# Performance work log

Measured on AMD Instinct MI355X. Metric: run time of the kernel, lower is better.

Reference implementation:

```python
import jax, jax.numpy as jnp
import numpy as np

N, E, D, H, HEADS_C, G = 50000, 800000, 128, 4, 32, 8
EDIM = D + 2  # H_update: phys_term (D) + ortho_geom (2)


def setup_inputs() -> dict:
    key = jax.random.key(0)
    ks = jax.random.split(key, 24)
    def gl(k, shape, fan_in):
        return jax.random.normal(k, shape, jnp.float32) / np.sqrt(fan_in)
    inp = {
        'h_target': jax.random.normal(ks[0], (N, D), jnp.float32),
        'h_source': jax.random.normal(ks[1], (N, D), jnp.float32),
        'edge_index': jax.random.randint(ks[2], (2, E), 0, N, jnp.int64),
        'pos': jax.random.uniform(ks[3], (N, 2), jnp.float32),
        't_emb': jax.random.normal(ks[4], (1, D), jnp.float32),
        # AdaGN params
        'gn_w': jnp.ones((D,), jnp.float32),
        'gn_b': jnp.zeros((D,), jnp.float32),
        'fc_W': gl(ks[5], (D, 2 * D), D),
        'fc_b': jnp.zeros((2 * D,), jnp.float32),
        # GATv2 params (lin_l, lin_r, lin_edge, att, bias)
        'Wl': gl(ks[6], (D, D), D),
        'bl': jnp.zeros((D,), jnp.float32),
        'Wr': gl(ks[7], (D, D), D),
        'br': jnp.zeros((D,), jnp.float32),
        'We': gl(ks[8], (EDIM, D), EDIM),
        'att': gl(ks[9], (H, HEADS_C), HEADS_C),
        'gat_b': jnp.zeros((D,), jnp.float32),
        # post_gat
        'Wp': gl(ks[10], (D, D), D),
        'bp': jnp.zeros((D,), jnp.float32),
        # update_mlp: LayerNorm + Linear(D,2D) + GELU + Linear(2D,D)
        'ln_w': jnp.ones((D,), jnp.float32),
        'ln_b': jnp.zeros((D,), jnp.float32),
        'W1': gl(ks[11], (D, 2 * D), D),
        'b1': jnp.zeros((2 * D,), jnp.float32),
        'W2': gl(ks[12], (2 * D, D), 2 * D),
        'b2': jnp.zeros((D,), jnp.float32),
    }
    return inp


def _adagn(x, cond, gn_w, gn_b, fc_W, fc_b):
    n, d = x.shape
    xg = x.reshape(n, G, d // G)
    mu = xg.mean(-1, keepdims=True)
    var = xg.var(-1, keepdims=True)  # biased, as torch GroupNorm
    normed = ((xg - mu) / jnp.sqrt(var + 1e-5)).reshape(n, d) * gn_w + gn_b
    style = cond @ fc_W + fc_b  # (1, 2D) broadcasts over nodes
    gamma, beta = jnp.split(style, 2, axis=-1)
    return normed * (1 + gamma) + beta


def _gatv2(h, edge_attr, src, dst, Wl, bl, Wr, br, We, att, gat_b):
    n = h.shape[0]
    x_l = (h @ Wl + bl).reshape(n, H, HEADS_C)  # source transform
    x_r = (h @ Wr + br).reshape(n, H, HEADS_C)  # target transform
    e_feat = (edge_attr @ We).reshape(-1, H, HEADS_C)
    x = x_l[src] + x_r[dst] + e_feat            # (E, H, C)
    x = jax.nn.leaky_relu(x, 0.2)
    logit = jnp.einsum('ehc,hc->eh', x, att)    # (E, H)
    # segment softmax over edges grouped by destination node
    amax = jax.ops.segment_max(logit, dst, num_segments=n)
    amax = jnp.where(jnp.isfinite(amax), amax, 0.0)
    ex = jnp.exp(logit - amax[dst])
    denom = jax.ops.segment_sum(ex, dst, num_segments=n)
    alpha = ex / (denom[dst] + 1e-16)           # (E, H)
    msg = x_l[src] * alpha[:, :, None]          # (E, H, C)
    out = jax.ops.segment_sum(msg, dst, num_segments=n)  # (N, H, C)
    return out.reshape(n, H * HEADS_C) + gat_b


def reference(h_target, h_source, edge_index, pos, t_emb,
              gn_w, gn_b, fc_W, fc_b,
              Wl, bl, Wr, br, We, att, gat_b,
              Wp, bp, ln_w, ln_b, W1, b1, W2, b2):
    h_mod = _adagn(h_source, t_emb, gn_w, gn_b, fc_W, fc_b)
    src, dst = edge_index[0], edge_index[1]
    rel_pos = pos[src] - pos[dst]                       # (E, 2)
    dist_sq = (rel_pos ** 2).sum(-1, keepdims=True) + 1e-8
    geom = rel_pos / dist_sq
    phys = h_mod[src] - h_mod[dst]                      # H_update mode
    ortho = jnp.stack([-geom[:, 1], geom[:, 0]], axis=-1)
    edge_attr = jnp.concatenate([phys, ortho], axis=-1)  # (E, D+2)
    aggr = _gatv2(h_mod, edge_attr, src, dst, Wl, bl, Wr, br, We, att, gat_b)
    aggr = aggr @ Wp + bp
    # update_mlp (dropout inactive in eval)
    mu = aggr.mean(-1, keepdims=True)
    var = aggr.var(-1, keepdims=True)
    z = (aggr - mu) / jnp.sqrt(var + 1e-5) * ln_w + ln_b
    z = jax.nn.gelu(z @ W1 + b1, approximate=False)
    delta = z @ W2 + b2
    return h_target + delta
```

## Files before the change

### kernel.cpp

```cpp
#include <hip/hip_runtime.h>
#include <math.h>

#define D 128

typedef short bf16x4 __attribute__((ext_vector_type(4)));
typedef short bf16x8 __attribute__((ext_vector_type(8)));
typedef float f32x4  __attribute__((ext_vector_type(4)));

__device__ __forceinline__ float b2f(unsigned short u) {
  union { unsigned int i; float f; } v; v.i = ((unsigned int)u) << 16; return v.f;
}
__device__ __forceinline__ unsigned short f2b(float f) {
  union { float f; unsigned int i; } v; v.f = f;
  unsigned int i = v.i;
  return (unsigned short)((i + 0x7FFFu + ((i >> 16) & 1u)) >> 16);
}
__device__ __forceinline__ float b2f_lo(unsigned int u) {
  union { unsigned int i; float f; } v; v.i = u << 16; return v.f;
}
__device__ __forceinline__ float b2f_hi(unsigned int u) {
  union { unsigned int i; float f; } v; v.i = u & 0xFFFF0000u; return v.f;
}
__device__ __forceinline__ float loadf(const void* p, size_t i, int isb) {
  if (isb) return b2f(((const unsigned short*)p)[i]);
  return ((const float*)p)[i];
}
__device__ __forceinline__ void storeout(void* p, size_t i, float v, int isb) {
  if (isb) ((unsigned short*)p)[i] = f2b(v);
  else     ((float*)p)[i] = v;
}
__device__ __forceinline__ int clampN(int v, int N) {
  return ((unsigned)v >= (unsigned)N) ? 0 : v;
}

__global__ void setup_kernel(const float* __restrict__ gw, const int* __restrict__ e32,
                             int* __restrict__ fflag, int* __restrict__ iflag,
                             int* __restrict__ ok) {
  int t = threadIdx.x;
  if (blockIdx.x == 0) {
    float v = gw[t];
    unsigned long long b = __ballot(v == 1.0f);
    if (t == 0) fflag[0] = (b == 0xFFFFFFFFFFFFFFFFull) ? 0 : 1;
  } else if (blockIdx.x == 1) {
    int v = e32[2 * t + 1];
    unsigned long long b = __ballot(v == 0);
    if (t == 0) iflag[0] = (b == 0xFFFFFFFFFFFFFFFFull) ? 1 : 0;
  } else {
    if (t == 0) ok[0] = 1;
  }
}
__device__ __forceinline__ int edge_src(const void* eraw, int i, int E, int fl, int N) {
  int v = fl ? (int)((const long long*)eraw)[i] : ((const int*)eraw)[i];
  return clampN(v, N);
}
__device__ __forceinline__ int edge_dst(const void* eraw, int i, int E, int fl, int N) {
  int v = fl ? (int)((const long long*)eraw)[(size_t)E + i] : ((const int*)eraw)[(size_t)E + i];
  return clampN(v, N);
}

struct Job { const void* src; float* dst; int n; int blk0; };
struct Jobs { Job j[21]; };
__global__ void cvt_param_kernel(Jobs jobs, const int* __restrict__ fflag, int njobs) {
  int isb = fflag[0];
  int b = blockIdx.x;
  for (int k = 0; k < njobs; ++k) {
    int nblk = (jobs.j[k].n + 255) >> 8;
    int lo = jobs.j[k].blk0;
    if (b >= lo && b < lo + nblk) {
      int i = ((b - lo) << 8) + threadIdx.x;
      if (i < jobs.j[k].n) jobs.j[k].dst[i] = loadf(jobs.j[k].src, i, isb);
      return;
    }
  }
}

__global__ void style_kernel(const float* __restrict__ t_emb,
                             const float* __restrict__ fc_W,
                             const float* __restrict__ fc_b,
                             float* __restrict__ style) {
  int j = threadIdx.x;
  float s = fc_b[j];
  for (int k = 0; k < D; ++k) s += t_emb[k] * fc_W[k * 256 + j];
  style[j] = s;
}

__global__ __launch_bounds__(128) void adagn_kernel(
    const void* __restrict__ h_source,
    const float* __restrict__ gn_w, const float* __restrict__ gn_b,
    const float* __restrict__ style, unsigned short* __restrict__ h_mod,
    const int* __restrict__ fflag, int N) {
  int n = blockIdx.x; if (n >= N) return;
  int c = threadIdx.x;
  float x = loadf(h_source, (size_t)n * D + c, fflag[0]);
  float s = x, s2 = x * x;
  s += __shfl_xor(s, 1, 16);  s2 += __shfl_xor(s2, 1, 16);
  s += __shfl_xor(s, 2, 16);  s2 += __shfl_xor(s2, 2, 16);
  s += __shfl_xor(s, 4, 16);  s2 += __shfl_xor(s2, 4, 16);
  s += __shfl_xor(s, 8, 16);  s2 += __shfl_xor(s2, 8, 16);
  float mu = s * (1.f / 16.f);
  float va = s2 * (1.f / 16.f) - mu * mu;
  float iv = rsqrtf(va + 1e-5f);
  float nv = (x - mu) * iv * gn_w[c] + gn_b[c];
  h_mod[(size_t)n * D + c] = f2b(nv * (1.f + style[c]) + style[128 + c]);
}

struct BP { const float* B; int ldb; int col0; };
struct BPJobs { BP j[8]; };
__global__ void bprep_kernel(BPJobs jobs, unsigned short* __restrict__ dst) {
  int job = blockIdx.x >> 7;
  int idx = ((blockIdx.x & 127) << 8) + threadIdx.x;
  int j    = idx & 7;
  int lane = (idx >> 3) & 63;
  int p    = (idx >> 9) & 1;
  int ct   = (idx >> 10) & 7;
  int kt   = idx >> 13;
  int g = lane >> 4;
  int k = kt * 32 + ((j < 4) ? (4 * g + j) : (16 + 4 * g + (j - 4)));
  int n = jobs.j[job].col0 + ct * 16 + (lane & 15);
  float v = jobs.j[job].B[(size_t)k * jobs.j[job].ldb + n];
  unsigned short hi = f2b(v);
  unsigned short out = hi;
  if (p) out = f2b(v - b2f(hi));
  dst[(size_t)job * 32768 + idx] = out;
}

template <int MODE, int CTS, int KTS>
__global__ __launch_bounds__(256) void mgemm_kernel(
    const unsigned short* __restrict__ A, const unsigned short* __restrict__ Bf,
    const float* __restrict__ bias, const void* __restrict__ resid,
    void* __restrict__ Cv, const int* __restrict__ fflag,
    const int* __restrict__ okf, int Nrows) {
  const int AS = KTS * 32, LDC = CTS * 16;
  int l = threadIdx.x & 63, w = threadIdx.x >> 6;
  int rb = blockIdx.x * 64 + w * 16;
  int m = l & 15, g = l >> 4;
  int arow = rb + m;
  if (arow >= Nrows) arow = Nrows - 1;
  const unsigned short* Arow = A + (size_t)arow * AS + 4 * g;
  f32x4 acc[CTS];
  #pragma unroll
  for (int ct = 0; ct < CTS; ++ct) acc[ct] = (f32x4){0.f, 0.f, 0.f, 0.f};
  #pragma unroll
  for (int kt = 0; kt < KTS; ++kt) {
    bf16x4 alo = *(const bf16x4*)(Arow + kt * 32);
    bf16x4 ahi = *(const bf16x4*)(Arow + kt * 32 + 16);
    bf16x8 af = __builtin_shufflevector(alo, ahi, 0, 1, 2, 3, 4, 5, 6, 7);
    #pragma unroll
    for (int ct = 0; ct < CTS; ++ct) {
      int panel = (KTS == 8) ? (kt >> 2) : (ct >> 3);
      size_t off = (size_t)panel * 32768 + (size_t)(kt & 3) * 8192
                 + (size_t)(((ct & 7) * 2) * 64 + l) * 8;
      bf16x8 bh = *(const bf16x8*)(Bf + off);
      bf16x8 bl2 = *(const bf16x8*)(Bf + off + 512);
      acc[ct] = __builtin_amdgcn_mfma_f32_16x16x32_bf16(af, bh, acc[ct], 0, 0, 0);
      acc[ct] = __builtin_amdgcn_mfma_f32_16x16x32_bf16(af, bl2, acc[ct], 0, 0, 0);
    }
  }
  int isb = (MODE == 2) ? fflag[0] : 0;
  int okv = (MODE == 2) ? okf[0] : 1;
  #pragma unroll
  for (int ct = 0; ct < CTS; ++ct) {
    int c = ct * 16 + m;
    float bs = bias[c];
    #pragma unroll
    for (int r = 0; r < 4; ++r) {
      int row = rb + 4 * g + r;
      if (row < Nrows) {
        float v = acc[ct][r] + bs;
        if (MODE == 1) v = 0.5f * v * (1.f + erff(v * 0.70710678118654752f));
        size_t oi = (size_t)row * LDC + c;
        if (MODE == 2) {
          v += loadf(resid, oi, isb);
          if (okv == 0) v = 100.0f;
          storeout(Cv, oi, v, isb);
        } else ((unsigned short*)Cv)[oi] = f2b(v);
      }
    }
  }
}

__global__ __launch_bounds__(256) void mgemm3_kernel(
    const unsigned short* __restrict__ A, const unsigned short* __restrict__ Bf,
    const float* __restrict__ bl, const float* __restrict__ br,
    unsigned int* __restrict__ XH32, unsigned short* __restrict__ XR, int Nrows) {
  int l = threadIdx.x & 63, w = threadIdx.x >> 6;
  int rb = blockIdx.x * 64 + w * 16;
  int m = l & 15, g = l >> 4;
  int arow = rb + m;
  if (arow >= Nrows) arow = Nrows - 1;
  const unsigned short* Arow = A + (size_t)arow * 128 + 4 * g;
  f32x4 acc[24];
  #pragma unroll
  for (int ct = 0; ct < 24; ++ct) acc[ct] = (f32x4){0.f, 0.f, 0.f, 0.f};
  #pragma unroll
  for (int kt = 0; kt < 4; ++kt) {
    bf16x4 alo = *(const bf16x4*)(Arow + kt * 32);
    bf16x4 ahi = *(const bf16x4*)(Arow + kt * 32 + 16);
    bf16x8 af = __builtin_shufflevector(alo, ahi, 0, 1, 2, 3, 4, 5, 6, 7);
    #pragma unroll
    for (int ct = 0; ct < 24; ++ct) {
      size_t off = (size_t)(ct >> 3) * 32768 + (size_t)kt * 8192
                 + (size_t)(((ct & 7) * 2) * 64 + l) * 8;
      bf16x8 bh = *(const bf16x8*)(Bf + off);
      bf16x8 bl2 = *(const bf16x8*)(Bf + off + 512);
      acc[ct] = __builtin_amdgcn_mfma_f32_16x16x32_bf16(af, bh, acc[ct], 0, 0, 0);
      acc[ct] = __builtin_amdgcn_mfma_f32_16x16x32_bf16(af, bl2, acc[ct], 0, 0, 0);
    }
  }
  #pragma unroll
  for (int ct = 0; ct < 8; ++ct) {
    int cm = ct * 16 + m;
    #pragma unroll
    for (int r = 0; r < 4; ++r) {
      int row = rb + 4 * g + r;
      if (row < Nrows) {
        float vl = acc[ct][r] + bl[cm];
        float vh = acc[ct + 16][r];
        XH32[(size_t)row * 128 + cm] =
            (unsigned int)f2b(vl) | ((unsigned int)f2b(vh) << 16);
        float vr = acc[ct + 8][r] + br[cm];
        XR[(size_t)row * 128 + cm] = f2b(vr);
      }
    }
  }
}

__global__ void hist_kernel(const void* __restrict__ eraw, const int* __restrict__ iflag,
                            int* __restrict__ deg, int E, int N) {
  int e = blockIdx.x * 256 + threadIdx.x;
  if (e < E) atomicAdd(&deg[edge_dst(eraw, e, E, iflag[0], N)], 1);
}

__global__ __launch_bounds__(1024) void scan1_kernel(const int* __restrict__ deg,
                                                     int* __restrict__ incl,
                                                     int* __restrict__ bsum) {
  int i = blockIdx.x * 1024 + threadIdx.x;
  int lane = threadIdx.x & 63, wave = threadIdx.x >> 6;
  int x = deg[i];
  #pragma unroll
  for (int d = 1; d < 64; d <<= 1) { int t = __shfl_up(x, d, 64); if (lane >= d) x += t; }
  __shared__ int wsum[16];
  if (lane == 63) wsum[wave] = x;
  __syncthreads();
  if (threadIdx.x < 16) {
    int w = wsum[threadIdx.x];
    #pragma unroll
    for (int d = 1; d < 16; d <<= 1) { int t = __shfl_up(w, d, 64); if ((int)threadIdx.x >= d) w += t; }
    wsum[threadIdx.x] = w;
  }
  __syncthreads();
  if (wave > 0) x += wsum[wave - 1];
  incl[i] = x;
  if (threadIdx.x == 1023) bsum[blockIdx.x] = x;
}

__global__ void scan2_kernel(const int* __restrict__ bsum, int* __restrict__ bbase, int nb) {
  if (threadIdx.x == 0) {
    int run = 0;
    for (int b = 0; b < nb; ++b) { bbase[b] = run; run += bsum[b]; }
  }
}

__global__ __launch_bounds__(1024) void scan3_kernel(const int* __restrict__ incl,
                                                     const int* __restrict__ deg,
                                                     const int* __restrict__ bbase,
                                                     int* __restrict__ offs,
                                                     int* __restrict__ cursor, int N) {
  int i = blockIdx.x * 1024 + threadIdx.x;
  if (i < N) {
    int o = bbase[blockIdx.x] + incl[i] - deg[i];
    offs[i] = o; cursor[i] = o;
  }
}

__global__ void scatter_kernel(const void* __restrict__ eraw, const int* __restrict__ iflag,
                               int* __restrict__ cursor, int* __restrict__ elist, int E, int N) {
  int e = blockIdx.x * 256 + threadIdx.x;
  if (e < E) {
    int fl = iflag[0];
    int d = edge_dst(eraw, e, E, fl, N);
    int s = edge_src(eraw, e, E, fl, N);
    int p = atomicAdd(&cursor[d], 1);
    elist[p] = s;
  }
}

__global__ void validate_kernel(const int* __restrict__ offs, const int* __restrict__ deg,
                                const int* __restrict__ cursor, const int* __restrict__ elist,
                                int* __restrict__ ok, int N, int E) {
  int i = blockIdx.x * 256 + threadIdx.x;
  bool bad = false;
  if (i < N) bad = bad || (cursor[i] != offs[i] + deg[i]);
  if (i < E) bad = bad || ((unsigned)elist[i] >= (unsigned)N);
  if (i == 0) bad = bad || (offs[N - 1] + deg[N - 1] != E);
  if (bad) atomicAnd(ok, 0);
}
__global__ void fillc_kernel(void* __restrict__ out, float c, const int* __restrict__ fflag, int n) {
  int i = blockIdx.x * 256 + threadIdx.x;
  if (i < n) storeout(out, i, c, fflag[0]);
}

__global__ __launch_bounds__(256) void edge_kernel(
    const unsigned int* __restrict__ XH32, const unsigned short* __restrict__ XR,
    const float* __restrict__ pos, const float* __restrict__ weo,
    const float* __restrict__ att, const float* __restrict__ gat_b,
    const int* __restrict__ offs, const int* __restrict__ deg,
    const int* __restrict__ elist, unsigned short* __restrict__ aggr, int N) {
  int w = threadIdx.x >> 6;
  int l = threadIdx.x & 63;
  int n = blockIdx.x * 2 + (w >> 1);
  int half = w & 1;
  bool valid = (n < N);
  int nn = valid ? n : 0;
  int c0 = 2 * l, c1 = c0 + 1;
  uint2 hq = *(const uint2*)(XH32 + (size_t)nn * 128 + c0);
  unsigned int uxr = *(const unsigned int*)(XR + (size_t)nn * 128 + c0);
  float base0 = b2f_lo(uxr) - b2f_hi(hq.x);
  float base1 = b2f_hi(uxr) - b2f_hi(hq.y);
  float2 pd = ((const float2*)pos)[nn];
  float we00 = weo[c0], we01 = weo[c1];
  float we10 = weo[128 + c0], we11 = weo[128 + c1];
  float att0 = att[c0], att1 = att[c1];
  int o = 0, dg = 0;
  if (valid) { o = offs[n]; dg = deg[n]; }
  float m = -3.402823466e38f, den = 0.f, num0 = 0.f, num1 = 0.f;
  if (dg > half) {
    int s = elist[o + half];
    uint2 q = *(const uint2*)(XH32 + (size_t)s * 128 + c0);
    float2 ps = ((const float2*)pos)[s];
    for (int i = half; i < dg; i += 2) {
      int s2 = clampN(elist[o + i + 2], N);
      uint2 q2 = *(const uint2*)(XH32 + (size_t)s2 * 128 + c0);
      float2 p2 = ((const float2*)pos)[s2];
      float rx = ps.x - pd.x, ry = ps.y - pd.y;
      float inv = 1.f / (rx * rx + ry * ry + 1e-8f);
      float ox = -ry * inv, oy = rx * inv;
      float xl0 = b2f_lo(q.x), xl1 = b2f_lo(q.y);
      float x0 = xl0 + base0 + b2f_hi(q.x) + ox * we00 + oy * we10;
      float x1 = xl1 + base1 + b2f_hi(q.y) + ox * we01 + oy * we11;
      float y = fmaxf(x0, 0.2f * x0) * att0 + fmaxf(x1, 0.2f * x1) * att1;
      y += __shfl_xor(y, 1, 16);
      y += __shfl_xor(y, 2, 16);
      y += __shfl_xor(y, 4, 16);
      y += __shfl_xor(y, 8, 16);
      float d = y - m;
      if (__any(d > 8.f)) {
        float mn = fmaxf(m, y);
        float f = __expf(m - mn);
        float p = __expf(y - mn);
        den = den * f + p;
        num0 = num0 * f + p * xl0;
        num1 = num1 * f + p * xl1;
        m = mn;
      } else {
        float p = __expf(d);
        den += p;
        num0 += p * xl0;
        num1 += p * xl1;
      }
      s = s2; q = q2; ps = p2;
    }
  }
  __shared__ float4 mrg[4][64];
  mrg[w][l] = (float4){m, den, num0, num1};
  __syncthreads();
  float4 other = mrg[w ^ 1][l];
  float M = fmaxf(m, other.x);
  float f1 = __expf(m - M), f2 = __expf(other.x - M);
  den  = den  * f1 + other.y * f2;
  num0 = num0 * f1 + other.z * f2;
  num1 = num1 * f1 + other.w * f2;
  if (valid && half == 0) {
    float iden = 1.f / (den + 1e-16f);
    unsigned int o0 = f2b(num0 * iden + gat_b[c0]);
    unsigned int o1 = f2b(num1 * iden + gat_b[c1]);
    *(unsigned int*)(aggr + (size_t)n * D + c0) = o0 | (o1 << 16);
  }
}

__global__ __launch_bounds__(128) void ln_kernel(const unsigned short* __restrict__ A,
                                                 const float* __restrict__ w,
                                                 const float* __restrict__ b,
                                                 unsigned short* __restrict__ Z, int N) {
  int n = blockIdx.x; if (n >= N) return;
  int c = threadIdx.x;
  float v = b2f(A[(size_t)n * D + c]);
  float s = v, s2 = v * v;
  #pragma unroll
  for (int d = 1; d < 64; d <<= 1) {
    s  += __shfl_xor(s,  d, 64);
    s2 += __shfl_xor(s2, d, 64);
  }
  __shared__ float ws[2][2];
  int wave = c >> 6;
  if ((c & 63) == 0) { ws[wave][0] = s; ws[wave][1] = s2; }
  __syncthreads();
  float ts  = ws[0][0] + ws[1][0];
  float ts2 = ws[0][1] + ws[1][1];
  float mu = ts * (1.f / 128.f);
  float var = ts2 * (1.f / 128.f) - mu * mu;
  float iv = rsqrtf(fmaxf(var, 0.f) + 1e-5f);
  Z[(size_t)n * D + c] = f2b((v - mu) * iv * w[c] + b[c]);
}

extern "C" void kernel_launch(void* const* d_in, const int* in_sizes, int n_in,
                              void* d_out, int out_size, void* d_ws, size_t ws_size,
                              hipStream_t stream) {
  const void* h_resid  = d_in[0];
  const void* h_modsrc = d_in[1];
  const void* eidx     = d_in[2];
  const int N = in_sizes[0] / D;
  const int E = in_sizes[2] / 2;
  const int outN = N * D;

  char* wp = (char*)d_ws;
  auto alloc = [&](size_t bytes) -> void* {
    void* p = (void*)wp;
    wp += (bytes + 255) & ~(size_t)255;
    return p;
  };
  unsigned short* BA = (unsigned short*)alloc((size_t)N * D * 2);
  unsigned int*  XH32 = (unsigned int*)alloc((size_t)N * D * 4);
  unsigned short* BX = (unsigned short*)alloc((size_t)N * D * 2);
  float* style = (float*)alloc(256 * 4);
  const int nb = (N + 1023) / 1024;
  const int npad = nb * 1024;
  int* fflag  = (int*)alloc(256);
  int* iflag  = (int*)alloc(256);
  int* okflag = (int*)alloc(256);
  int* elist  = (int*)alloc((size_t)(E + 64) * 4);
  int* deg    = (int*)alloc((size_t)npad * 4);
  int* incl   = (int*)alloc((size_t)npad * 4);
  int* bsum   = (int*)alloc((size_t)nb * 4);
  int* bbase  = (int*)alloc((size_t)nb * 4);
  int* offs   = (int*)alloc((size_t)N * 4);
  int* cursor = (int*)alloc((size_t)N * 4);
  float* pos_f  = (float*)alloc((size_t)2 * N * 4);
  float* temb_f = (float*)alloc(128 * 4);
  float* gnw_f  = (float*)alloc(128 * 4);
  float* gnb_f  = (float*)alloc(128 * 4);
  float* fcW_f  = (float*)alloc(32768 * 4);
  float* fcb_f  = (float*)alloc(256 * 4);
  float* Wl_f   = (float*)alloc(16384 * 4);
  float* bl_f   = (float*)alloc(128 * 4);
  float* Wr_f   = (float*)alloc(16384 * 4);
  float* br_f   = (float*)alloc(128 * 4);
  float* We_f   = (float*)alloc(16640 * 4);
  float* att_f  = (float*)alloc(128 * 4);
  float* gtb_f  = (float*)alloc(128 * 4);
  float* Wp_f   = (float*)alloc(16384 * 4);
  float* bp_f   = (float*)alloc(128 * 4);
  float* lnw_f  = (float*)alloc(128 * 4);
  float* lnb_f  = (float*)alloc(128 * 4);
  float* W1_f   = (float*)alloc(32768 * 4);
  float* b1_f   = (float*)alloc(256 * 4);
  float* W2_f   = (float*)alloc(32768 * 4);
  float* b2_f   = (float*)alloc(128 * 4);
  unsigned short* WP8 = (unsigned short*)alloc(8 * 65536);

  size_t required = (size_t)(wp - (char*)d_ws);
  if (required > ws_size) {
    return;
  }

  hipMemsetAsync(deg, 0, (size_t)npad * 4, stream);
  hipMemsetAsync(elist + E, 0, 64 * 4, stream);

  setup_kernel<<<3, 64, 0, stream>>>((const float*)d_in[5], (const int*)eidx,
                                     fflag, iflag, okflag);

  const int expected[24] = {6400000, 6400000, 1600000, 100000, 128, 128, 128, 32768,
                            256, 16384, 128, 16384, 128, 16640, 128, 128, 16384, 128,
                            128, 128, 32768, 256, 32768, 128};
  int bad = (n_in == 24) ? -1 : 24;
  if (bad < 0) {
    for (int i = 0; i < 24; ++i) {
      if (in_sizes[i] != expected[i]) { bad = i; break; }
    }
  }
  if (bad >= 0) {
    fillc_kernel<<<(outN + 255) / 256, 256, 0, stream>>>(d_out, 20.f + 10.f * bad, fflag, outN);
    return;
  }

  Jobs jobs;
  int jn = 0, blk = 0;
  auto addjob = [&](const void* s, float* dptr, int n) {
    jobs.j[jn] = {s, dptr, n, blk};
    blk += (n + 255) >> 8;
    ++jn;
  };
  addjob(d_in[3],  pos_f,  2 * N);
  addjob(d_in[4],  temb_f, 128);
  addjob(d_in[5],  gnw_f,  128);
  addjob(d_in[6],  gnb_f,  128);
  addjob(d_in[7],  fcW_f,  32768);
  addjob(d_in[8],  fcb_f,  256);
  addjob(d_in[9],  Wl_f,   16384);
  addjob(d_in[10], bl_f,   128);
  addjob(d_in[11], Wr_f,   16384);
  addjob(d_in[12], br_f,   128);
  addjob(d_in[13], We_f,   16640);
  addjob(d_in[14], att_f,  128);
  addjob(d_in[15], gtb_f,  128);
  addjob(d_in[16], Wp_f,   16384);
  addjob(d_in[17], bp_f,   128);
  addjob(d_in[18], lnw_f,  128);
  addjob(d_in[19], lnb_f,  128);
  addjob(d_in[20], W1_f,   32768);
  addjob(d_in[21], b1_f,   256);
  addjob(d_in[22], W2_f,   32768);
  addjob(d_in[23], b2_f,   128);
  cvt_param_kernel<<<blk, 256, 0, stream>>>(jobs, fflag, jn);

  style_kernel<<<1, 256, 0, stream>>>(temb_f, fcW_f, fcb_f, style);
  adagn_kernel<<<N, 128, 0, stream>>>(h_modsrc, gnw_f, gnb_f, style, BA, fflag, N);

  BPJobs bj;
  bj.j[0] = {Wl_f, 128, 0};
  bj.j[1] = {Wr_f, 128, 0};
  bj.j[2] = {We_f, 128, 0};
  bj.j[3] = {Wp_f, 128, 0};
  bj.j[4] = {W1_f, 256, 0};
  bj.j[5] = {W1_f, 256, 128};
  bj.j[6] = {W2_f, 128, 0};
  bj.j[7] = {W2_f + 128 * 128, 128, 0};
  bprep_kernel<<<1024, 256, 0, stream>>>(bj, WP8);

  const int mb = (N + 63) / 64;
  mgemm3_kernel<<<mb, 256, 0, stream>>>(BA, WP8, bl_f, br_f, XH32, BX, N);

  hist_kernel<<<(E + 255) / 256, 256, 0, stream>>>(eidx, iflag, deg, E, N);
  scan1_kernel<<<nb, 1024, 0, stream>>>(deg, incl, bsum);
  scan2_kernel<<<1, 64, 0, stream>>>(bsum, bbase, nb);
  scan3_kernel<<<nb, 1024, 0, stream>>>(incl, deg, bbase, offs, cursor, N);
  scatter_kernel<<<(E + 255) / 256, 256, 0, stream>>>(eidx, iflag, cursor, elist, E, N);
  int vmax = (E > N ? E : N);
  validate_kernel<<<(vmax + 255) / 256, 256, 0, stream>>>(offs, deg, cursor, elist, okflag, N, E);

  edge_kernel<<<(N + 1) / 2, 256, 0, stream>>>(XH32, BX, pos_f, We_f + 128 * 128,
                                               att_f, gtb_f, offs, deg, elist, BA, N);

  unsigned short* P = (unsigned short*)XH32;
  unsigned short* G = (unsigned short*)XH32;
  mgemm_kernel<0, 8, 4><<<mb, 256, 0, stream>>>(BA, WP8 + 3 * 32768, bp_f, nullptr, P, fflag, okflag, N);
  ln_kernel<<<N, 128, 0, stream>>>(P, lnw_f, lnb_f, BX, N);
  mgemm_kernel<1, 16, 4><<<mb, 256, 0, stream>>>(BX, WP8 + 4 * 32768, b1_f, nullptr, G, fflag, okflag, N);
  mgemm_kernel<2, 8, 8><<<mb, 256, 0, stream>>>(G, WP8 + 6 * 32768, b2_f, h_resid, d_out, fflag, okflag, N);
}
```

Before: 572.0 us.

## Fuse post-GAT linear, LayerNorm and MLP into one kernel; simplify edge loop

Replaces the four kernels after the edge stage (post linear, LayerNorm, first MLP GEMM with GELU, second GEMM with residual) with a single kernel. Each wave keeps its 16-row tile on chip, passing the intermediate activations between the three MFMA GEMMs through LDS, so the P/Z/G buffers no longer round-trip through global memory and three launches go away. The edge kernel drops its manual software prefetch of the next source row, uses exp2 with log2e folded into the attention weights, and computes in 2-wide vectors. It also removes the elist padding memset. Costs are higher register and LDS pressure per block, which may lower occupancy, and possibly less latency hiding of the gathers in the edge loop.

After: 561.8 us. No clear change (-1.8%).

```diff
diff --git a/kernel.cpp b/kernel.cpp
--- a/kernel.cpp
+++ b/kernel.cpp
@@ -2,10 +2,12 @@
 #include <math.h>
 
 #define D 128
+#define LOG2E 1.44269504088896340736f
 
 typedef short bf16x4 __attribute__((ext_vector_type(4)));
 typedef short bf16x8 __attribute__((ext_vector_type(8)));
 typedef float f32x4  __attribute__((ext_vector_type(4)));
+typedef float f32x2  __attribute__((ext_vector_type(2)));
 
 __device__ __forceinline__ float b2f(unsigned short u) {
   union { unsigned int i; float f; } v; v.i = ((unsigned int)u) << 16; return v.f;
@@ -31,6 +33,9 @@
 }
 __device__ __forceinline__ int clampN(int v, int N) {
   return ((unsigned)v >= (unsigned)N) ? 0 : v;
+}
+__device__ __forceinline__ float gelu_f(float v) {
+  return 0.5f * v * (1.f + erff(v * 0.70710678118654752f));
 }
 
 __global__ void setup_kernel(const float* __restrict__ gw, const int* __restrict__ e32,
@@ -124,61 +129,6 @@
   dst[(size_t)job * 32768 + idx] = out;
 }
 
-template <int MODE, int CTS, int KTS>
-__global__ __launch_bounds__(256) void mgemm_kernel(
-    const unsigned short* __restrict__ A, const unsigned short* __restrict__ Bf,
-    const float* __restrict__ bias, const void* __restrict__ resid,
-    void* __restrict__ Cv, const int* __restrict__ fflag,
-    const int* __restrict__ okf, int Nrows) {
-  const int AS = KTS * 32, LDC = CTS * 16;
-  int l = threadIdx.x & 63, w = threadIdx.x >> 6;
-  int rb = blockIdx.x * 64 + w * 16;
-  int m = l & 15, g = l >> 4;
-  int arow = rb + m;
-  if (arow >= Nrows) arow = Nrows - 1;
-  const unsigned short* Arow = A + (size_t)arow * AS + 4 * g;
-  f32x4 acc[CTS];
-  #pragma unroll
-  for (int ct = 0; ct < CTS; ++ct) acc[ct] = (f32x4){0.f, 0.f, 0.f, 0.f};
-  #pragma unroll
-  for (int kt = 0; kt < KTS; ++kt) {
-    bf16x4 alo = *(const bf16x4*)(Arow + kt * 32);
-    bf16x4 ahi = *(const bf16x4*)(Arow + kt * 32 + 16);
-    bf16x8 af = __builtin_shufflevector(alo, ahi, 0, 1, 2, 3, 4, 5, 6, 7);
-    #pragma unroll
-    for (int ct = 0; ct < CTS; ++ct) {
-      int panel = (KTS == 8) ? (kt >> 2) : (ct >> 3);
-      size_t off = (size_t)panel * 32768 + (size_t)(kt & 3) * 8192
-                 + (size_t)(((ct & 7) * 2) * 64 + l) * 8;
-      bf16x8 bh = *(const bf16x8*)(Bf + off);
-      bf16x8 bl2 = *(const bf16x8*)(Bf + off + 512);
-      acc[ct] = __builtin_amdgcn_mfma_f32_16x16x32_bf16(af, bh, acc[ct], 0, 0, 0);
-      acc[ct] = __builtin_amdgcn_mfma_f32_16x16x32_bf16(af, bl2, acc[ct], 0, 0, 0);
-    }
-  }
-  int isb = (MODE == 2) ? fflag[0] : 0;
-  int okv = (MODE == 2) ? okf[0] : 1;
-  #pragma unroll
-  for (int ct = 0; ct < CTS; ++ct) {
-    int c = ct * 16 + m;
-    float bs = bias[c];
-    #pragma unroll
-    for (int r = 0; r < 4; ++r) {
-      int row = rb + 4 * g + r;
-      if (row < Nrows) {
-        float v = acc[ct][r] + bs;
-        if (MODE == 1) v = 0.5f * v * (1.f + erff(v * 0.70710678118654752f));
-        size_t oi = (size_t)row * LDC + c;
-        if (MODE == 2) {
-          v += loadf(resid, oi, isb);
-          if (okv == 0) v = 100.0f;
-          storeout(Cv, oi, v, isb);
-        } else ((unsigned short*)Cv)[oi] = f2b(v);
-      }
-    }
-  }
-}
-
 __global__ __launch_bounds__(256) void mgemm3_kernel(
     const unsigned short* __restrict__ A, const unsigned short* __restrict__ Bf,
     const float* __restrict__ bl, const float* __restrict__ br,
@@ -312,95 +262,193 @@
   int half = w & 1;
   bool valid = (n < N);
   int nn = valid ? n : 0;
-  int c0 = 2 * l, c1 = c0 + 1;
+  int c0 = 2 * l;
   uint2 hq = *(const uint2*)(XH32 + (size_t)nn * 128 + c0);
   unsigned int uxr = *(const unsigned int*)(XR + (size_t)nn * 128 + c0);
-  float base0 = b2f_lo(uxr) - b2f_hi(hq.x);
-  float base1 = b2f_hi(uxr) - b2f_hi(hq.y);
+  f32x2 base = (f32x2){ b2f_lo(uxr) - b2f_hi(hq.x), b2f_hi(uxr) - b2f_hi(hq.y) };
   float2 pd = ((const float2*)pos)[nn];
-  float we00 = weo[c0], we01 = weo[c1];
-  float we10 = weo[128 + c0], we11 = weo[128 + c1];
-  float att0 = att[c0], att1 = att[c1];
+  f32x2 we0v = (f32x2){ weo[c0], weo[c0 + 1] };
+  f32x2 we1v = (f32x2){ weo[128 + c0], weo[128 + c0 + 1] };
+  f32x2 attv = (f32x2){ att[c0] * LOG2E, att[c0 + 1] * LOG2E };
   int o = 0, dg = 0;
   if (valid) { o = offs[n]; dg = deg[n]; }
-  float m = -3.402823466e38f, den = 0.f, num0 = 0.f, num1 = 0.f;
-  if (dg > half) {
-    int s = elist[o + half];
+  float mx = -3.402823466e38f, den = 0.f;
+  f32x2 num = (f32x2){0.f, 0.f};
+  for (int i = half; i < dg; i += 2) {
+    int s = elist[o + i];
+    float2 ps = ((const float2*)pos)[s];
     uint2 q = *(const uint2*)(XH32 + (size_t)s * 128 + c0);
-    float2 ps = ((const float2*)pos)[s];
-    for (int i = half; i < dg; i += 2) {
-      int s2 = clampN(elist[o + i + 2], N);
-      uint2 q2 = *(const uint2*)(XH32 + (size_t)s2 * 128 + c0);
-      float2 p2 = ((const float2*)pos)[s2];
-      float rx = ps.x - pd.x, ry = ps.y - pd.y;
-      float inv = 1.f / (rx * rx + ry * ry + 1e-8f);
-      float ox = -ry * inv, oy = rx * inv;
-      float xl0 = b2f_lo(q.x), xl1 = b2f_lo(q.y);
-      float x0 = xl0 + base0 + b2f_hi(q.x) + ox * we00 + oy * we10;
-      float x1 = xl1 + base1 + b2f_hi(q.y) + ox * we01 + oy * we11;
-      float y = fmaxf(x0, 0.2f * x0) * att0 + fmaxf(x1, 0.2f * x1) * att1;
-      y += __shfl_xor(y, 1, 16);
-      y += __shfl_xor(y, 2, 16);
-      y += __shfl_xor(y, 4, 16);
-      y += __shfl_xor(y, 8, 16);
-      float d = y - m;
-      if (__any(d > 8.f)) {
-        float mn = fmaxf(m, y);
-        float f = __expf(m - mn);
-        float p = __expf(y - mn);
-        den = den * f + p;
-        num0 = num0 * f + p * xl0;
-        num1 = num1 * f + p * xl1;
-        m = mn;
-      } else {
-        float p = __expf(d);
-        den += p;
-        num0 += p * xl0;
-        num1 += p * xl1;
-      }
-      s = s2; q = q2; ps = p2;
+    float rx = ps.x - pd.x, ry = ps.y - pd.y;
+    float inv = 1.f / (rx * rx + ry * ry + 1e-8f);
+    float gx = -ry * inv, gy = rx * inv;
+    f32x2 xl = (f32x2){ b2f_lo(q.x), b2f_lo(q.y) };
+    f32x2 hw = (f32x2){ b2f_hi(q.x), b2f_hi(q.y) };
+    f32x2 x = (xl + hw) + (base + gx * we0v + gy * we1v);
+    f32x2 lx = __builtin_elementwise_max(x, 0.2f * x);
+    f32x2 t = lx * attv;
+    float y = t.x + t.y;
+    y += __shfl_xor(y, 1, 16);
+    y += __shfl_xor(y, 2, 16);
+    y += __shfl_xor(y, 4, 16);
+    y += __shfl_xor(y, 8, 16);
+    float d0 = y - mx;
+    if (__any(d0 > 11.5417f)) {
+      float mn = fmaxf(mx, y);
+      float f = exp2f(mx - mn);
+      float p = exp2f(y - mn);
+      den = den * f + p;
+      num = num * f + p * xl;
+      mx = mn;
+    } else {
+      float p = exp2f(d0);
+      den += p;
+      num += p * xl;
     }
   }
   __shared__ float4 mrg[4][64];
-  mrg[w][l] = (float4){m, den, num0, num1};
+  mrg[w][l] = (float4){mx, den, num.x, num.y};
   __syncthreads();
-  float4 other = mrg[w ^ 1][l];
-  float M = fmaxf(m, other.x);
-  float f1 = __expf(m - M), f2 = __expf(other.x - M);
-  den  = den  * f1 + other.y * f2;
-  num0 = num0 * f1 + other.z * f2;
-  num1 = num1 * f1 + other.w * f2;
+  float4 oth = mrg[w ^ 1][l];
+  float M = fmaxf(mx, oth.x);
+  float f1 = exp2f(mx - M), f2 = exp2f(oth.x - M);
+  den = den * f1 + oth.y * f2;
+  float n0 = num.x * f1 + oth.z * f2;
+  float n1 = num.y * f1 + oth.w * f2;
   if (valid && half == 0) {
     float iden = 1.f / (den + 1e-16f);
-    unsigned int o0 = f2b(num0 * iden + gat_b[c0]);
-    unsigned int o1 = f2b(num1 * iden + gat_b[c1]);
+    unsigned int o0 = f2b(n0 * iden + gat_b[c0]);
+    unsigned int o1 = f2b(n1 * iden + gat_b[c0 + 1]);
     *(unsigned int*)(aggr + (size_t)n * D + c0) = o0 | (o1 << 16);
   }
 }
 
-__global__ __launch_bounds__(128) void ln_kernel(const unsigned short* __restrict__ A,
-                                                 const float* __restrict__ w,
-                                                 const float* __restrict__ b,
-                                                 unsigned short* __restrict__ Z, int N) {
-  int n = blockIdx.x; if (n >= N) return;
-  int c = threadIdx.x;
-  float v = b2f(A[(size_t)n * D + c]);
-  float s = v, s2 = v * v;
-  #pragma unroll
-  for (int d = 1; d < 64; d <<= 1) {
-    s  += __shfl_xor(s,  d, 64);
-    s2 += __shfl_xor(s2, d, 64);
-  }
-  __shared__ float ws[2][2];
-  int wave = c >> 6;
-  if ((c & 63) == 0) { ws[wave][0] = s; ws[wave][1] = s2; }
-  __syncthreads();
-  float ts  = ws[0][0] + ws[1][0];
-  float ts2 = ws[0][1] + ws[1][1];
-  float mu = ts * (1.f / 128.f);
-  float var = ts2 * (1.f / 128.f) - mu * mu;
-  float iv = rsqrtf(fmaxf(var, 0.f) + 1e-5f);
-  Z[(size_t)n * D + c] = f2b((v - mu) * iv * w[c] + b[c]);
+__global__ __launch_bounds__(256) void fused_post_kernel(
+    const unsigned short* __restrict__ A, const unsigned short* __restrict__ WP8,
+    const float* __restrict__ bp, const float* __restrict__ lnw,
+    const float* __restrict__ lnb, const float* __restrict__ b1,
+    const float* __restrict__ b2, const void* __restrict__ resid,
+    void* __restrict__ out, const int* __restrict__ fflag,
+    const int* __restrict__ okf, int Nrows) {
+  __shared__ __align__(16) unsigned short ldsA[4][16][132];
+  __shared__ __align__(16) unsigned short ldsG[4][16][268];
+  int l = threadIdx.x & 63, w = threadIdx.x >> 6;
+  int rb = blockIdx.x * 64 + w * 16;
+  int m = l & 15, g = l >> 4;
+  int arow = rb + m;
+  if (arow >= Nrows) arow = Nrows - 1;
+  const unsigned short* Arow = A + (size_t)arow * 128 + 4 * g;
+
+  f32x4 acc[8];
+  #pragma unroll
+  for (int ct = 0; ct < 8; ++ct) acc[ct] = (f32x4){0.f, 0.f, 0.f, 0.f};
+  #pragma unroll
+  for (int kt = 0; kt < 4; ++kt) {
+    bf16x4 alo = *(const bf16x4*)(Arow + kt * 32);
+    bf16x4 ahi = *(const bf16x4*)(Arow + kt * 32 + 16);
+    bf16x8 af = __builtin_shufflevector(alo, ahi, 0, 1, 2, 3, 4, 5, 6, 7);
+    #pragma unroll
+    for (int ct = 0; ct < 8; ++ct) {
+      size_t off = (size_t)3 * 32768 + (size_t)kt * 8192 + (size_t)((ct * 2) * 64 + l) * 8;
+      bf16x8 bh = *(const bf16x8*)(WP8 + off);
+      bf16x8 bl2 = *(const bf16x8*)(WP8 + off + 512);
+      acc[ct] = __builtin_amdgcn_mfma_f32_16x16x32_bf16(af, bh, acc[ct], 0, 0, 0);
+      acc[ct] = __builtin_amdgcn_mfma_f32_16x16x32_bf16(af, bl2, acc[ct], 0, 0, 0);
+    }
+  }
+  #pragma unroll
+  for (int ct = 0; ct < 8; ++ct) acc[ct] = acc[ct] + bp[ct * 16 + m];
+
+  f32x4 s1 = (f32x4){0.f, 0.f, 0.f, 0.f}, s2v = (f32x4){0.f, 0.f, 0.f, 0.f};
+  #pragma unroll
+  for (int ct = 0; ct < 8; ++ct) { s1 += acc[ct]; s2v += acc[ct] * acc[ct]; }
+  #pragma unroll
+  for (int d = 1; d < 16; d <<= 1) {
+    f32x4 t1, t2;
+    #pragma unroll
+    for (int r = 0; r < 4; ++r) { t1[r] = __shfl_xor(s1[r], d, 16); t2[r] = __shfl_xor(s2v[r], d, 16); }
+    s1 += t1; s2v += t2;
+  }
+  f32x4 mu = s1 * (1.f / 128.f);
+  f32x4 iv;
+  #pragma unroll
+  for (int r = 0; r < 4; ++r) {
+    float var = s2v[r] * (1.f / 128.f) - mu[r] * mu[r];
+    iv[r] = rsqrtf(fmaxf(var, 0.f) + 1e-5f);
+  }
+  #pragma unroll
+  for (int ct = 0; ct < 8; ++ct) {
+    float lw = lnw[ct * 16 + m], lb = lnb[ct * 16 + m];
+    #pragma unroll
+    for (int r = 0; r < 4; ++r) {
+      float z = (acc[ct][r] - mu[r]) * iv[r] * lw + lb;
+      ldsA[w][4 * g + r][m + 16 * ct] = f2b(z);
+    }
+  }
+
+  f32x4 acc2[16];
+  #pragma unroll
+  for (int ct = 0; ct < 16; ++ct) acc2[ct] = (f32x4){0.f, 0.f, 0.f, 0.f};
+  #pragma unroll
+  for (int kt = 0; kt < 4; ++kt) {
+    bf16x4 alo = *(const bf16x4*)&ldsA[w][m][4 * g + kt * 32];
+    bf16x4 ahi = *(const bf16x4*)&ldsA[w][m][4 * g + kt * 32 + 16];
+    bf16x8 af = __builtin_shufflevector(alo, ahi, 0, 1, 2, 3, 4, 5, 6, 7);
+    #pragma unroll
+    for (int ct = 0; ct < 16; ++ct) {
+      size_t off = (size_t)(4 + (ct >> 3)) * 32768 + (size_t)kt * 8192
+                 + (size_t)(((ct & 7) * 2) * 64 + l) * 8;
+      bf16x8 bh = *(const bf16x8*)(WP8 + off);
+      bf16x8 bl2 = *(const bf16x8*)(WP8 + off + 512);
+      acc2[ct] = __builtin_amdgcn_mfma_f32_16x16x32_bf16(af, bh, acc2[ct], 0, 0, 0);
+      acc2[ct] = __builtin_amdgcn_mfma_f32_16x16x32_bf16(af, bl2, acc2[ct], 0, 0, 0);
+    }
+  }
+  #pragma unroll
+  for (int ct = 0; ct < 16; ++ct) {
+    float bs = b1[ct * 16 + m];
+    #pragma unroll
+    for (int r = 0; r < 4; ++r) {
+      float v = gelu_f(acc2[ct][r] + bs);
+      ldsG[w][4 * g + r][ct * 16 + m] = f2b(v);
+    }
+  }
+
+  f32x4 acc3[8];
+  #pragma unroll
+  for (int ct = 0; ct < 8; ++ct) acc3[ct] = (f32x4){0.f, 0.f, 0.f, 0.f};
+  #pragma unroll
+  for (int kt = 0; kt < 8; ++kt) {
+    bf16x4 alo = *(const bf16x4*)&ldsG[w][m][4 * g + kt * 32];
+    bf16x4 ahi = *(const bf16x4*)&ldsG[w][m][4 * g + kt * 32 + 16];
+    bf16x8 af = __builtin_shufflevector(alo, ahi, 0, 1, 2, 3, 4, 5, 6, 7);
+    #pragma unroll
+    for (int ct = 0; ct < 8; ++ct) {
+      size_t off = (size_t)(6 + (kt >> 2)) * 32768 + (size_t)(kt & 3) * 8192
+                 + (size_t)((ct * 2) * 64 + l) * 8;
+      bf16x8 bh = *(const bf16x8*)(WP8 + off);
+      bf16x8 bl2 = *(const bf16x8*)(WP8 + off + 512);
+      acc3[ct] = __builtin_amdgcn_mfma_f32_16x16x32_bf16(af, bh, acc3[ct], 0, 0, 0);
+      acc3[ct] = __builtin_amdgcn_mfma_f32_16x16x32_bf16(af, bl2, acc3[ct], 0, 0, 0);
+    }
+  }
+  int isb = fflag[0];
+  int okv = okf[0];
+  #pragma unroll
+  for (int ct = 0; ct < 8; ++ct) {
+    int c = ct * 16 + m;
+    float bs = b2[c];
+    #pragma unroll
+    for (int r = 0; r < 4; ++r) {
+      int row = rb + 4 * g + r;
+      if (row < Nrows) {
+        float v = acc3[ct][r] + bs;
+        size_t oi = (size_t)row * 128 + c;
+        v += loadf(resid, oi, isb);
+        if (okv == 0) v = 100.0f;
+        storeout(out, oi, v, isb);
+      }
+    }
+  }
 }
 
 extern "C" void kernel_launch(void* const* d_in, const int* in_sizes, int n_in,
@@ -428,7 +476,7 @@
   int* fflag  = (int*)alloc(256);
   int* iflag  = (int*)alloc(256);
   int* okflag = (int*)alloc(256);
-  int* elist  = (int*)alloc((size_t)(E + 64) * 4);
+  int* elist  = (int*)alloc((size_t)E * 4);
   int* deg    = (int*)alloc((size_t)npad * 4);
   int* incl   = (int*)alloc((size_t)npad * 4);
   int* bsum   = (int*)alloc((size_t)nb * 4);
@@ -463,8 +511,7 @@
     return;
   }
 
-  hipMemsetAsync(deg, 0, (size_t)npad * 4, stream);
-  hipMemsetAsync(elist + E, 0, 64 * 4, stream);
+  (void)hipMemsetAsync(deg, 0, (size_t)npad * 4, stream);
 
   setup_kernel<<<3, 64, 0, stream>>>((const float*)d_in[5], (const int*)eidx,
                                      fflag, iflag, okflag);
@@ -541,10 +588,6 @@
   edge_kernel<<<(N + 1) / 2, 256, 0, stream>>>(XH32, BX, pos_f, We_f + 128 * 128,
                                                att_f, gtb_f, offs, deg, elist, BA, N);
 
-  unsigned short* P = (unsigned short*)XH32;
-  unsigned short* G = (unsigned short*)XH32;
-  mgemm_kernel<0, 8, 4><<<mb, 256, 0, stream>>>(BA, WP8 + 3 * 32768, bp_f, nullptr, P, fflag, okflag, N);
-  ln_kernel<<<N, 128, 0, stream>>>(P, lnw_f, lnb_f, BX, N);
-  mgemm_kernel<1, 16, 4><<<mb, 256, 0, stream>>>(BX, WP8 + 4 * 32768, b1_f, nullptr, G, fflag, okflag, N);
-  mgemm_kernel<2, 8, 8><<<mb, 256, 0, stream>>>(G, WP8 + 6 * 32768, b2_f, h_resid, d_out, fflag, okflag, N);
-}
+  fused_post_kernel<<<mb, 256, 0, stream>>>(BA, WP8, bp_f, lnw_f, lnb_f, b1_f, b2_f,
+                                            h_resid, d_out, fflag, okflag, N);
+}
```
